# Kernel optimization log

Hardware: AMD Instinct MI355X
Metric: run time of the kernel (lower is better)

The kernel has to match this reference:

```python
import jax, jax.numpy as jnp
import numpy as np
from jax import lax

EPS = 1e-5
K = 7
G = 4


def _dwconv_bn(x, w, g, b, m, v):
    # depthwise 3x3, pad 1, then BN (eval mode with running stats)
    C = x.shape[1]
    y = lax.conv_general_dilated(x, w, (1, 1), [(1, 1), (1, 1)],
                                 feature_group_count=C,
                                 dimension_numbers=('NCHW', 'OIHW', 'NCHW'))
    scale = (g / jnp.sqrt(v + EPS))[None, :, None, None]
    return (y - m[None, :, None, None]) * scale + b[None, :, None, None]


def _proj(t, pw1, pb1, pw2, pb2):
    # 1x1 conv -> GELU(exact) -> 1x1 conv, on small spatial maps
    h = jnp.einsum('bchw,oc->bohw', t, pw1) + pb1[None, :, None, None]
    h = jax.nn.gelu(h, approximate=False)
    return jnp.einsum('bchw,oc->bohw', h, pw2) + pb2[None, :, None, None]


def setup_inputs() -> dict:
    key = jax.random.key(0)
    ks = jax.random.split(key, 17)
    B, C, H, W = 16, 256, 56, 56
    r = C // 4
    inp = {
        'x1': jax.random.normal(ks[0], (B, C, H, W), jnp.float32),
        'dw1_w': jax.random.normal(ks[1], (C, 1, 3, 3), jnp.float32) * 0.1,
        'dw1_g': jax.random.uniform(ks[2], (C,), jnp.float32, 0.5, 1.5),
        'dw1_b': jax.random.normal(ks[3], (C,), jnp.float32) * 0.1,
        'dw1_m': jax.random.normal(ks[4], (C,), jnp.float32) * 0.1,
        'dw1_v': jax.random.uniform(ks[5], (C,), jnp.float32, 0.5, 1.5),
        'dw2_w': jax.random.normal(ks[6], (C, 1, 3, 3), jnp.float32) * 0.1,
        'dw2_g': jax.random.uniform(ks[7], (C,), jnp.float32, 0.5, 1.5),
        'dw2_b': jax.random.normal(ks[8], (C,), jnp.float32) * 0.1,
        'dw2_m': jax.random.normal(ks[9], (C,), jnp.float32) * 0.1,
        'dw2_v': jax.random.uniform(ks[10], (C,), jnp.float32, 0.5, 1.5),
        'weight1': jax.random.normal(ks[11], (G, C, K, K), jnp.float32) * 0.02,
        'bias1': jax.random.normal(ks[12], (G, C), jnp.float32) * 0.02,
        'pw1': jax.random.normal(ks[13], (r, C), jnp.float32) * 0.05,
        'pb1': jax.random.normal(ks[14], (r,), jnp.float32) * 0.05,
        'pw2': jax.random.normal(ks[15], (C * G, r), jnp.float32) * 0.05,
        'pb2': jax.random.normal(ks[16], (C * G,), jnp.float32) * 0.05,
    }
    return inp


def reference(x1, dw1_w, dw1_g, dw1_b, dw1_m, dw1_v,
              dw2_w, dw2_g, dw2_b, dw2_m, dw2_v,
              weight1, bias1, pw1, pb1, pw2, pb2):
    B, C, H, W = x1.shape
    # gated fuse: relu6(dw1(x)) * dw2(x)
    a = jnp.clip(_dwconv_bn(x1, dw1_w, dw1_g, dw1_b, dw1_m, dw1_v), 0.0, 6.0)
    x_fuse = a * _dwconv_bn(x1, dw2_w, dw2_g, dw2_b, dw2_m, dw2_v)

    # adaptive avg pool to (K,K): H,W multiples of K -> uniform block means
    pooled = x_fuse.reshape(B, C, K, H // K, K, W // K).mean(axis=(3, 5))

    # dynamic kernel: proj -> softmax over groups -> weighted sum of weight1
    scale1 = _proj(pooled, pw1, pb1, pw2, pb2).reshape(B, G, C, K, K)
    scale1 = jax.nn.softmax(scale1, axis=1)
    w_dyn = jnp.sum(scale1 * weight1[None], axis=1)  # [B, C, K, K]

    # dynamic bias
    mean_x = x_fuse.mean(axis=(-2, -1), keepdims=True)  # [B, C, 1, 1]
    sb = _proj(mean_x, pw1, pb1, pw2, pb2).reshape(B, G, C)
    sb = jax.nn.softmax(sb, axis=1)
    b_dyn = jnp.sum(sb * bias1[None], axis=1)  # [B, C]

    # per-sample depthwise conv with dynamic weights
    pad = K // 2

    def per_sample(xi, wi):  # xi [C,H,W], wi [C,K,K]
        y = lax.conv_general_dilated(xi[None], wi[:, None], (1, 1),
                                     [(pad, pad), (pad, pad)],
                                     feature_group_count=C,
                                     dimension_numbers=('NCHW', 'OIHW', 'NCHW'))
        return y[0]

    out = jax.vmap(per_sample)(x_fuse, w_dyn)  # [B, C, H, W]
    return out + b_dyn[:, :, None, None]
```

## Files before the change

kernel.cpp:

```cpp
#include <hip/hip_runtime.h>
#include <math.h>

#define BATCH 16
#define CH 256
#define HW 56
#define NPIX (HW*HW)

typedef float f32x2 __attribute__((ext_vector_type(2)));

__device__ __forceinline__ void fuse_tile(
    const float* __restrict__ plane, int ty, int tx,
    const f32x2 w12[9], f32x2 sc12, f32x2 be12,
    float res[4][4])
{
    const int oy = 4 * ty;
    f32x2 y12a[4][4];
    #pragma unroll
    for (int a = 0; a < 4; a++)
        #pragma unroll
        for (int e = 0; e < 4; e++) y12a[a][e] = (f32x2){0.f, 0.f};

    #pragma unroll
    for (int iy = 0; iy < 6; iy++) {
        const int r    = oy - 1 + iy;
        const bool rok = (r >= 0) && (r < 56);
        const int rc   = rok ? r : 0;
        float rb[12];
        #pragma unroll
        for (int k = 0; k < 3; k++) {
            const int cx  = tx - 1 + k;
            const bool cv = (cx >= 0) && (cx < 14);
            const int cc2 = cv ? cx : 0;
            const bool ok = rok && cv;
            float4 v = *(const float4*)(plane + rc*56 + 4*cc2);
            rb[4*k+0] = ok ? v.x : 0.f;
            rb[4*k+1] = ok ? v.y : 0.f;
            rb[4*k+2] = ok ? v.z : 0.f;
            rb[4*k+3] = ok ? v.w : 0.f;
        }
        #pragma unroll
        for (int tyy = 0; tyy < 4; tyy++) {
            const int ky = iy - tyy;
            if (ky >= 0 && ky < 3) {
                #pragma unroll
                for (int e = 0; e < 4; e++)
                    #pragma unroll
                    for (int dj = 0; dj < 3; dj++) {
                        const float xv = rb[3 + e + dj];
                        const f32x2 xv2 = {xv, xv};
                        y12a[tyy][e] = __builtin_elementwise_fma(xv2, w12[ky*3+dj], y12a[tyy][e]);
                    }
            }
        }
    }
    #pragma unroll
    for (int tyy = 0; tyy < 4; tyy++)
        #pragma unroll
        for (int e = 0; e < 4; e++) {
            f32x2 yb = __builtin_elementwise_fma(y12a[tyy][e], sc12, be12);
            float a = fminf(fmaxf(yb.x, 0.f), 6.f);
            res[tyy][e] = a * yb.y;
        }
}

__global__ __launch_bounds__(256) void k1_pool(
    const float* __restrict__ x1,
    const float* __restrict__ dw1w, const float* __restrict__ g1, const float* __restrict__ b1,
    const float* __restrict__ m1, const float* __restrict__ v1,
    const float* __restrict__ dw2w, const float* __restrict__ g2, const float* __restrict__ b2,
    const float* __restrict__ m2, const float* __restrict__ v2,
    float* __restrict__ pooled)
{
    const int bc = blockIdx.x;
    const int c  = bc & 255;
    const int b  = bc >> 8;
    const int t  = threadIdx.x;

    __shared__ float part[196];

    f32x2 w12[9];
    #pragma unroll
    for (int k = 0; k < 9; k++) w12[k] = (f32x2){dw1w[c*9+k], dw2w[c*9+k]};
    const float sc1 = g1[c] * rsqrtf(v1[c] + 1e-5f);
    const float be1 = b1[c] - m1[c] * sc1;
    const float sc2 = g2[c] * rsqrtf(v2[c] + 1e-5f);
    const float be2 = b2[c] - m2[c] * sc2;
    const f32x2 sc12 = {sc1, sc2};
    const f32x2 be12 = {be1, be2};

    if (t < 196) {
        const int ty = t / 14, tx = t - ty * 14;
        float res[4][4];
        fuse_tile(x1 + (size_t)bc * NPIX, ty, tx, w12, sc12, be12, res);
        float s = 0.f;
        #pragma unroll
        for (int a = 0; a < 4; a++)
            #pragma unroll
            for (int e = 0; e < 4; e++) s += res[a][e];
        part[t] = s;
    }
    __syncthreads();
    if (t < 64) {
        float cs = 0.f;
        if (t < 49) {
            int ph = t / 7, pw = t - ph * 7;
            cs = part[(2*ph  )*14 + 2*pw] + part[(2*ph  )*14 + 2*pw + 1]
               + part[(2*ph+1)*14 + 2*pw] + part[(2*ph+1)*14 + 2*pw + 1];
            pooled[((size_t)(b * 50 + t)) * 256 + c] = cs * (1.f/64.f);
        }
        #pragma unroll
        for (int off = 32; off > 0; off >>= 1) cs += __shfl_down(cs, off);
        if (t == 0)
            pooled[((size_t)(b * 50 + 49)) * 256 + c] = cs * (1.f/64.f) * (1.f/49.f);
    }
}

__global__ __launch_bounds__(256) void k2a(
    const float* __restrict__ pooled,
    const float* __restrict__ pw1, const float* __restrict__ pb1,
    float* __restrict__ h)
{
    const int blk = blockIdx.x;
    const int b = blk / 50, p = blk - b * 50;
    const int t = threadIdx.x;

    __shared__ __attribute__((aligned(16))) float xs[272];

    xs[t + 4*(t>>6)] = pooled[((size_t)b * 50 + p) * 256 + t];
    __syncthreads();

    const int o = t >> 2, part = t & 3;
    const float4* w4 = (const float4*)(pw1 + o*256 + part*64);
    const float4* x4 = (const float4*)(xs + part*68);
    float acc = 0.f;
    #pragma unroll
    for (int i = 0; i < 16; i++) {
        float4 w = w4[i];
        float4 x = x4[i];
        acc += w.x*x.x + w.y*x.y + w.z*x.z + w.w*x.w;
    }
    acc += __shfl_xor(acc, 1);
    acc += __shfl_xor(acc, 2);
    if (part == 0) {
        float zv = acc + pb1[o];
        h[((size_t)b * 50 + p) * 64 + o] = 0.5f * zv * (1.f + erff(zv * 0.70710678118654752f));
    }
}

__global__ __launch_bounds__(256) void k2b(
    const float* __restrict__ h, const float* __restrict__ pw2, const float* __restrict__ pb2,
    const float* __restrict__ weight1, const float* __restrict__ bias1,
    float* __restrict__ w_dyn,
    float* __restrict__ b_dyn)
{
    const int b   = blockIdx.x;
    const int cch = blockIdx.y;
    const int t   = threadIdx.x;
    const int c_base = cch * 16;

    __shared__ float ht[64*52];
    __shared__ __attribute__((aligned(16))) float wg[16*64*4];

    const float* hp = h + (size_t)b * 50 * 64;
    for (int idx = t; idx < 800; idx += 256) {
        const int p = idx >> 4, k4 = idx & 15;
        float4 v = ((const float4*)(hp + p * 64))[k4];
        ht[(4*k4+0)*52 + p] = v.x;
        ht[(4*k4+1)*52 + p] = v.y;
        ht[(4*k4+2)*52 + p] = v.z;
        ht[(4*k4+3)*52 + p] = v.w;
    }
    for (int idx = t; idx < 1024; idx += 256) {
        const int r = idx >> 4, k4 = idx & 15;
        const int g = r >> 4, cl = r & 15;
        const int o2 = (g << 8) + c_base + cl;
        float4 v = ((const float4*)(pw2 + (size_t)o2 * 64))[k4];
        wg[((cl*64) + 4*k4+0)*4 + g] = v.x;
        wg[((cl*64) + 4*k4+1)*4 + g] = v.y;
        wg[((cl*64) + 4*k4+2)*4 + g] = v.z;
        wg[((cl*64) + 4*k4+3)*4 + g] = v.w;
    }
    __syncthreads();

    for (int idx = t; idx < 800; idx += 256) {
        const int cl = idx / 50, p = idx - cl * 50;
        const int c  = c_base + cl;
        float s0 = pb2[c], s1 = pb2[256 + c], s2 = pb2[512 + c], s3 = pb2[768 + c];
        const float4* wv = (const float4*)wg + cl * 64;
        #pragma unroll
        for (int k = 0; k < 64; k++) {
            const float x = ht[k*52 + p];
            const float4 w = wv[k];
            s0 += x * w.x; s1 += x * w.y; s2 += x * w.z; s3 += x * w.w;
        }
        float mx = fmaxf(fmaxf(s0, s1), fmaxf(s2, s3));
        float e0 = expf(s0-mx), e1 = expf(s1-mx), e2 = expf(s2-mx), e3 = expf(s3-mx);
        float inv = 1.f / (e0+e1+e2+e3);
        e0 *= inv; e1 *= inv; e2 *= inv; e3 *= inv;
        if (p < 49) {
            float wvv = e0*weight1[(0*256+c)*49+p] + e1*weight1[(1*256+c)*49+p]
                      + e2*weight1[(2*256+c)*49+p] + e3*weight1[(3*256+c)*49+p];
            w_dyn[((size_t)b*256 + c)*49 + p] = wvv;
        } else {
            b_dyn[b*256 + c] = e0*bias1[c] + e1*bias1[256+c] + e2*bias1[512+c] + e3*bias1[768+c];
        }
    }
}

#define SWZ(row, chunk) ((row)*64 + 4*((chunk) ^ (((row)>>2)&7)))
__global__ __launch_bounds__(256) void k3_dyn(
    const float* __restrict__ x1,
    const float* __restrict__ dw1w, const float* __restrict__ g1, const float* __restrict__ b1,
    const float* __restrict__ m1, const float* __restrict__ v1,
    const float* __restrict__ dw2w, const float* __restrict__ g2, const float* __restrict__ b2,
    const float* __restrict__ m2, const float* __restrict__ v2,
    const float* __restrict__ w_dyn, const float* __restrict__ b_dyn,
    float* __restrict__ out)
{
    const int bc = blockIdx.x;
    const int c  = bc & 255;
    const int t  = threadIdx.x;
    __shared__ __attribute__((aligned(16))) float halo[62*64];

    f32x2 w12[9];
    #pragma unroll
    for (int k = 0; k < 9; k++) w12[k] = (f32x2){dw1w[c*9+k], dw2w[c*9+k]};
    const float sc1 = g1[c] * rsqrtf(v1[c] + 1e-5f);
    const float be1 = b1[c] - m1[c] * sc1;
    const float sc2 = g2[c] * rsqrtf(v2[c] + 1e-5f);
    const float be2 = b2[c] - m2[c] * sc2;
    const f32x2 sc12 = {sc1, sc2};
    const f32x2 be12 = {be1, be2};
    float wk[49];
    const float* wp = w_dyn + (size_t)bc * 49;
    #pragma unroll
    for (int k = 0; k < 49; k++) wk[k] = wp[k];
    const float bias = b_dyn[bc];

    if (t < 208) {
        int row, c4;
        if (t < 48)       { row = t >> 4;             c4 = t & 15; }
        else if (t < 96)  { row = 59 + ((t-48) >> 4); c4 = (t-48) & 15; }
        else if (t < 152) { row = 3 + (t - 96);       c4 = 0; }
        else              { row = 3 + (t - 152);      c4 = 15; }
        *(float4*)&halo[SWZ(row, c4)] = make_float4(0.f, 0.f, 0.f, 0.f);
    }

    const int ty = t / 14, tx = t - ty * 14;
    if (t < 196) {
        float res[4][4];
        fuse_tile(x1 + (size_t)bc * NPIX, ty, tx, w12, sc12, be12, res);
        #pragma unroll
        for (int tyy = 0; tyy < 4; tyy++) {
            float4 r4; r4.x=res[tyy][0]; r4.y=res[tyy][1]; r4.z=res[tyy][2]; r4.w=res[tyy][3];
            *(float4*)&halo[SWZ(4*ty + tyy + 3, tx + 1)] = r4;
        }
    }
    __syncthreads();

    if (t < 196) {
        const int oy = ty * 4, ox = tx * 4;
        float acc[4][4];
        #pragma unroll
        for (int a = 0; a < 4; a++)
            #pragma unroll
            for (int bb = 0; bb < 4; bb++) acc[a][bb] = bias;

        #pragma unroll
        for (int iy = 0; iy < 10; iy++) {
            const int row = oy + iy;
            float4 a  = *(const float4*)&halo[SWZ(row, tx    )];
            float4 b  = *(const float4*)&halo[SWZ(row, tx + 1)];
            float4 cc = *(const float4*)&halo[SWZ(row, tx + 2)];
            float rowv[12];
            rowv[0]=a.x; rowv[1]=a.y; rowv[2]=a.z; rowv[3]=a.w;
            rowv[4]=b.x; rowv[5]=b.y; rowv[6]=b.z; rowv[7]=b.w;
            rowv[8]=cc.x; rowv[9]=cc.y; rowv[10]=cc.z; rowv[11]=cc.w;
            #pragma unroll
            for (int tyy = 0; tyy < 4; tyy++) {
                const int ky = iy - tyy;
                if (ky >= 0 && ky < 7) {
                    #pragma unroll
                    for (int txx = 0; txx < 4; txx++)
                        #pragma unroll
                        for (int kx = 0; kx < 7; kx++)
                            acc[tyy][txx] += rowv[1+txx+kx] * wk[ky*7+kx];
                }
            }
        }
        float* op = out + (size_t)bc * NPIX;
        #pragma unroll
        for (int tyy = 0; tyy < 4; tyy++) {
            float4 r4; r4.x = acc[tyy][0]; r4.y = acc[tyy][1]; r4.z = acc[tyy][2]; r4.w = acc[tyy][3];
            *(float4*)(op + (oy+tyy)*56 + ox) = r4;
        }
    }
}

extern "C" void kernel_launch(void* const* d_in, const int* in_sizes, int n_in,
                              void* d_out, int out_size, void* d_ws, size_t ws_size,
                              hipStream_t stream) {
    const float* x1    = (const float*)d_in[0];
    const float* dw1w  = (const float*)d_in[1];
    const float* dw1g  = (const float*)d_in[2];
    const float* dw1b  = (const float*)d_in[3];
    const float* dw1m  = (const float*)d_in[4];
    const float* dw1v  = (const float*)d_in[5];
    const float* dw2w  = (const float*)d_in[6];
    const float* dw2g  = (const float*)d_in[7];
    const float* dw2b  = (const float*)d_in[8];
    const float* dw2m  = (const float*)d_in[9];
    const float* dw2v  = (const float*)d_in[10];
    const float* weight1 = (const float*)d_in[11];
    const float* bias1   = (const float*)d_in[12];
    const float* pw1     = (const float*)d_in[13];
    const float* pb1     = (const float*)d_in[14];
    const float* pw2     = (const float*)d_in[15];
    const float* pb2     = (const float*)d_in[16];

    float* out = (float*)d_out;
    float* ws  = (float*)d_ws;
    float* pooled = ws;
    float* h      = ws + 204800;
    float* w_dyn  = ws + 256000;
    float* b_dyn  = ws + 456704;

    k1_pool<<<BATCH*CH, 256, 0, stream>>>(x1, dw1w, dw1g, dw1b, dw1m, dw1v,
                                          dw2w, dw2g, dw2b, dw2m, dw2v, pooled);
    k2a<<<800, 256, 0, stream>>>(pooled, pw1, pb1, h);
    k2b<<<dim3(BATCH, 16), 256, 0, stream>>>(h, pw2, pb2, weight1, bias1, w_dyn, b_dyn);
    k3_dyn<<<BATCH*CH, 256, 0, stream>>>(x1, dw1w, dw1g, dw1b, dw1m, dw1v,
                                         dw2w, dw2g, dw2b, dw2m, dw2v,
                                         w_dyn, b_dyn, out);
}
```

Baseline: 183.1 us.

## Materialize fused dwconv activation in k1 instead of recomputing it in k3

k1 now writes the fused output of the two depthwise 3x3 convs with BN and activation to a workspace buffer while it computes the pooled sums. k3 loads that buffer into shared memory instead of running fuse_tile again on x1. This removes the duplicated 3x3 dwconv and BN arithmetic. In exchange it adds one full-tensor write and one full-tensor read of global memory, and it needs a larger workspace allocation.

```diff
diff --git a/kernel.cpp b/kernel.cpp
--- a/kernel.cpp
+++ b/kernel.cpp
@@ -69,7 +69,8 @@
     const float* __restrict__ m1, const float* __restrict__ v1,
     const float* __restrict__ dw2w, const float* __restrict__ g2, const float* __restrict__ b2,
     const float* __restrict__ m2, const float* __restrict__ v2,
-    float* __restrict__ pooled)
+    float* __restrict__ pooled,
+    float* __restrict__ xf)
 {
     const int bc = blockIdx.x;
     const int c  = bc & 255;
@@ -93,10 +94,13 @@
         float res[4][4];
         fuse_tile(x1 + (size_t)bc * NPIX, ty, tx, w12, sc12, be12, res);
         float s = 0.f;
-        #pragma unroll
-        for (int a = 0; a < 4; a++)
-            #pragma unroll
-            for (int e = 0; e < 4; e++) s += res[a][e];
+        float* fp = xf + (size_t)bc * NPIX;
+        #pragma unroll
+        for (int tyy = 0; tyy < 4; tyy++) {
+            float4 r4; r4.x=res[tyy][0]; r4.y=res[tyy][1]; r4.z=res[tyy][2]; r4.w=res[tyy][3];
+            *(float4*)(fp + (4*ty + tyy)*56 + 4*tx) = r4;
+            s += res[tyy][0] + res[tyy][1] + res[tyy][2] + res[tyy][3];
+        }
         part[t] = s;
     }
     __syncthreads();
@@ -208,29 +212,15 @@
 }
 
 #define SWZ(row, chunk) ((row)*64 + 4*((chunk) ^ (((row)>>2)&7)))
-__global__ __launch_bounds__(256) void k3_dyn(
-    const float* __restrict__ x1,
-    const float* __restrict__ dw1w, const float* __restrict__ g1, const float* __restrict__ b1,
-    const float* __restrict__ m1, const float* __restrict__ v1,
-    const float* __restrict__ dw2w, const float* __restrict__ g2, const float* __restrict__ b2,
-    const float* __restrict__ m2, const float* __restrict__ v2,
+__global__ __launch_bounds__(256) void k3_conv(
+    const float* __restrict__ xf,
     const float* __restrict__ w_dyn, const float* __restrict__ b_dyn,
     float* __restrict__ out)
 {
     const int bc = blockIdx.x;
-    const int c  = bc & 255;
     const int t  = threadIdx.x;
     __shared__ __attribute__((aligned(16))) float halo[62*64];
 
-    f32x2 w12[9];
-    #pragma unroll
-    for (int k = 0; k < 9; k++) w12[k] = (f32x2){dw1w[c*9+k], dw2w[c*9+k]};
-    const float sc1 = g1[c] * rsqrtf(v1[c] + 1e-5f);
-    const float be1 = b1[c] - m1[c] * sc1;
-    const float sc2 = g2[c] * rsqrtf(v2[c] + 1e-5f);
-    const float be2 = b2[c] - m2[c] * sc2;
-    const f32x2 sc12 = {sc1, sc2};
-    const f32x2 be12 = {be1, be2};
     float wk[49];
     const float* wp = w_dyn + (size_t)bc * 49;
     #pragma unroll
@@ -248,12 +238,11 @@
 
     const int ty = t / 14, tx = t - ty * 14;
     if (t < 196) {
-        float res[4][4];
-        fuse_tile(x1 + (size_t)bc * NPIX, ty, tx, w12, sc12, be12, res);
+        const float* fp = xf + (size_t)bc * NPIX;
         #pragma unroll
         for (int tyy = 0; tyy < 4; tyy++) {
-            float4 r4; r4.x=res[tyy][0]; r4.y=res[tyy][1]; r4.z=res[tyy][2]; r4.w=res[tyy][3];
-            *(float4*)&halo[SWZ(4*ty + tyy + 3, tx + 1)] = r4;
+            float4 v = *(const float4*)(fp + (4*ty + tyy)*56 + 4*tx);
+            *(float4*)&halo[SWZ(4*ty + tyy + 3, tx + 1)] = v;
         }
     }
     __syncthreads();
@@ -324,12 +313,11 @@
     float* h      = ws + 204800;
     float* w_dyn  = ws + 256000;
     float* b_dyn  = ws + 456704;
+    float* xf     = ws + 460800;
 
     k1_pool<<<BATCH*CH, 256, 0, stream>>>(x1, dw1w, dw1g, dw1b, dw1m, dw1v,
-                                          dw2w, dw2g, dw2b, dw2m, dw2v, pooled);
+                                          dw2w, dw2g, dw2b, dw2m, dw2v, pooled, xf);
     k2a<<<800, 256, 0, stream>>>(pooled, pw1, pb1, h);
     k2b<<<dim3(BATCH, 16), 256, 0, stream>>>(h, pw2, pb2, weight1, bias1, w_dyn, b_dyn);
-    k3_dyn<<<BATCH*CH, 256, 0, stream>>>(x1, dw1w, dw1g, dw1b, dw1m, dw1v,
-                                         dw2w, dw2g, dw2b, dw2m, dw2v,
-                                         w_dyn, b_dyn, out);
-}
+    k3_conv<<<BATCH*CH, 256, 0, stream>>>(xf, w_dyn, b_dyn, out);
+}
```

Measured after the change: 185.5 us. About the same (+1.3%).
